# Performance work log

Hardware: AMD Instinct MI355X
Metric: run time of the kernel (lower is better)

Reference implementation:

```python
import jax, jax.numpy as jnp
import numpy as np

# snntorch Leaky defaults / CFG constants
BETA = 0.9      # CFG.lif_beta
IAPP = 0.0      # CFG.Iapp
THR = 1.0       # snn.Leaky default threshold
SLOPE = 25.0    # surrogate.fast_sigmoid default slope


@jax.custom_vjp
def spike(x):
    # Heaviside spike with fast-sigmoid surrogate gradient
    return (x > 0).astype(x.dtype)

def _spike_fwd(x):
    return spike(x), x

def _spike_bwd(x, g):
    return (g / (SLOPE * jnp.abs(x) + 1.0) ** 2,)

spike.defvjp(_spike_fwd, _spike_bwd)


def setup_inputs() -> dict:
    key = jax.random.key(0)
    z = jax.random.normal(key, (32, 1024, 512), dtype=jnp.float32)
    return {"z": z}


def reference(z):
    # z: [B, T, H]; sequential LIF over time axis.
    # snntorch Leaky (reset='subtract'):
    #   reset = detach(V_prev > thr)
    #   V_k   = beta * V_prev + input_k - reset * thr
    #   spk_k = heaviside(V_k - thr)
    # Original loop: input at step k is z[:, k-1] + Iapp (noise std = 0.0).
    B, T, H = z.shape
    zt = jnp.transpose(z[:, :-1, :], (1, 0, 2))  # [T-1, B, H]
    V0 = jnp.zeros((B, H), dtype=z.dtype)

    def step(V, zin):
        reset = jax.lax.stop_gradient((V > THR).astype(V.dtype))
        Vn = BETA * V + (zin + IAPP) - reset * THR
        spk = spike(Vn - THR)
        return Vn, spk

    _, spks = jax.lax.scan(step, V0, zt)  # spks: [T-1, B, H]
    # T[:, 0, :] stays zero (loop starts at k=1)
    Tout = jnp.concatenate(
        [jnp.zeros((B, 1, H), dtype=z.dtype), jnp.transpose(spks, (1, 0, 2))],
        axis=1,
    )
    return Tout
```

## Files before the change

kernel.cpp:

```cpp
#include <hip/hip_runtime.h>


#define LIF_H 512
#define LIF_T 1024
#define CH 128
#define NCH 8
#define NPROD 4
#define NTHREADS (64 * (1 + NPROD))

#define GLDS(gptr, lptr)                                                     \
    __builtin_amdgcn_global_load_lds(                                        \
        (const __attribute__((address_space(1))) void*)(gptr),               \
        (__attribute__((address_space(3))) void*)(lptr), 16, 0, 0)

__global__ __launch_bounds__(NTHREADS, 1) void lif_kernel(const float* __restrict__ z,
                                                          float* __restrict__ out) {
    extern __shared__ float lds[];

    const int tid  = threadIdx.x;
    const int wave = tid >> 6;
    const int lane = tid & 63;
    const int bid  = blockIdx.x;
    const int b    = bid >> 3;
    const int h0   = (bid & 7) << 6;

    const float* zb = z   + b * (LIF_T * LIF_H) + h0;
    float*       ob = out + b * (LIF_T * LIF_H) + h0;

    if (wave == 0) {
        ob[lane] = 0.0f;
    } else {
        const int p = wave - 1;
#pragma unroll
        for (int j = 0; j < 8; ++j) {
            const int r0 = p * 32 + j * 4;
            GLDS(zb + (r0 + (lane >> 4)) * LIF_H + (lane & 15) * 4,
                 &lds[0 * (CH * 64) + r0 * 64]);
        }
#pragma unroll
        for (int j = 0; j < 8; ++j) {
            const int r0 = p * 32 + j * 4;
            GLDS(zb + (CH + r0 + (lane >> 4)) * LIF_H + (lane & 15) * 4,
                 &lds[1 * (CH * 64) + r0 * 64]);
        }
        __builtin_amdgcn_sched_barrier(0);
        asm volatile("s_waitcnt vmcnt(8)" ::: "memory");
    }
    __builtin_amdgcn_s_barrier();

    float V = 0.0f;
    float r = 0.0f;
    int cbuf = 0;

#define LDRB(rb, sub)                                                        \
    _Pragma("unroll")                                                        \
    for (int i = 0; i < 32; ++i) rb[i] = lb[((sub) * 32 + i) * 64 + lane];

#define CHAIN(rb, s0, N)                                                     \
    _Pragma("unroll")                                                        \
    for (int i = 0; i < (N); ++i) {                                          \
        const float u  = __fadd_rn(__fmul_rn(0.9f, V), rb[i]);               \
        const float Vn = __fsub_rn(u, r);                                    \
        const float sp = (Vn > 1.0f) ? 1.0f : 0.0f;                          \
        ob[((s0) + i + 1) * LIF_H + lane] = sp;                              \
        r = sp;                                                              \
        V = Vn;                                                              \
    }

#pragma unroll 1
    for (int c = 0; c < NCH; ++c) {
        if (wave > 0) {
            if (c + 2 < NCH) {
                const int p = wave - 1;
                int wbuf = cbuf + 2; if (wbuf >= 3) wbuf -= 3;
                float* dst = &lds[wbuf * (CH * 64)];
                const float* src = zb + (c + 2) * CH * LIF_H;
#pragma unroll
                for (int j = 0; j < 8; ++j) {
                    const int r0 = p * 32 + j * 4;
                    GLDS(src + (r0 + (lane >> 4)) * LIF_H + (lane & 15) * 4,
                         &dst[r0 * 64]);
                }
                __builtin_amdgcn_sched_barrier(0);
                asm volatile("s_waitcnt vmcnt(8)" ::: "memory");
            } else if (c + 1 < NCH) {
                asm volatile("s_waitcnt vmcnt(0)" ::: "memory");
            }
        } else {
            const float* lb = &lds[cbuf * (CH * 64)];
            const int s0 = c * CH;
            float rbA[32], rbB[32];
            LDRB(rbA, 0);
            LDRB(rbB, 1);
            __builtin_amdgcn_sched_barrier(0);
            CHAIN(rbA, s0 + 0, 32);
            LDRB(rbA, 2);
            __builtin_amdgcn_sched_barrier(0);
            CHAIN(rbB, s0 + 32, 32);
            LDRB(rbB, 3);
            __builtin_amdgcn_sched_barrier(0);
            CHAIN(rbA, s0 + 64, 32);
            __builtin_amdgcn_sched_barrier(0);
            if (c < NCH - 1) {
                CHAIN(rbB, s0 + 96, 32);
            } else {
                CHAIN(rbB, s0 + 96, 31);
            }
        }

        __builtin_amdgcn_s_barrier();
        cbuf = (cbuf == 2) ? 0 : cbuf + 1;
    }
}

extern "C" void kernel_launch(void* const* d_in, const int* in_sizes, int n_in,
                              void* d_out, int out_size, void* d_ws, size_t ws_size,
                              hipStream_t stream) {
    const float* z = (const float*)d_in[0];
    float* out = (float*)d_out;
    hipLaunchKernelGGL(lif_kernel, dim3(256), dim3(NTHREADS),
                       3 * CH * 64 * sizeof(float), stream, z, out);
}
```

Before: 113.4 us.

## Consolidate LIF blocks to 256 columns with four consumer waves and double buffering

Each block now covers 256 hidden columns instead of 64, with four consumer waves and eight producer waves, so the grid drops from 256 blocks to 64. The triple-buffered 128-row LDS pipeline becomes a double-buffered 64-row one, and producers fully drain their loads each phase. The aim is more recurrence chains per CU, fewer loads per thread and simpler buffer rotation. The cost is that three quarters of the CUs sit idle, prefetch runs only one chunk ahead, and there are twice as many block barriers.

Result: slower. 138.7 us (+22.3%).

```diff
diff --git a/kernel.cpp b/kernel.cpp
--- a/kernel.cpp
+++ b/kernel.cpp
@@ -3,10 +3,12 @@
 
 #define LIF_H 512
 #define LIF_T 1024
-#define CH 128
-#define NCH 8
-#define NPROD 4
-#define NTHREADS (64 * (1 + NPROD))
+#define CH 64
+#define NPH 16
+#define NCONS 4
+#define NPROD 8
+#define NTHREADS ((NCONS + NPROD) * 64)
+#define ROWF 256
 
 #define GLDS(gptr, lptr)                                                     \
     __builtin_amdgcn_global_load_lds(                                        \
@@ -21,40 +23,29 @@
     const int wave = tid >> 6;
     const int lane = tid & 63;
     const int bid  = blockIdx.x;
-    const int b    = bid >> 3;
-    const int h0   = (bid & 7) << 6;
+    const int b    = bid >> 1;
+    const int h0   = (bid & 1) << 8;
 
     const float* zb = z   + b * (LIF_T * LIF_H) + h0;
     float*       ob = out + b * (LIF_T * LIF_H) + h0;
 
-    if (wave == 0) {
-        ob[lane] = 0.0f;
+    if (wave < NCONS) {
+        ob[wave * 64 + lane] = 0.0f;
     } else {
-        const int p = wave - 1;
+        const int p = wave - NCONS;
 #pragma unroll
         for (int j = 0; j < 8; ++j) {
-            const int r0 = p * 32 + j * 4;
-            GLDS(zb + (r0 + (lane >> 4)) * LIF_H + (lane & 15) * 4,
-                 &lds[0 * (CH * 64) + r0 * 64]);
-        }
-#pragma unroll
-        for (int j = 0; j < 8; ++j) {
-            const int r0 = p * 32 + j * 4;
-            GLDS(zb + (CH + r0 + (lane >> 4)) * LIF_H + (lane & 15) * 4,
-                 &lds[1 * (CH * 64) + r0 * 64]);
+            const int r = p * 8 + j;
+            GLDS(zb + r * LIF_H + lane * 4, &lds[r * ROWF]);
         }
         __builtin_amdgcn_sched_barrier(0);
-        asm volatile("s_waitcnt vmcnt(8)" ::: "memory");
+        asm volatile("s_waitcnt vmcnt(0)" ::: "memory");
     }
     __builtin_amdgcn_s_barrier();
 
     float V = 0.0f;
     float r = 0.0f;
-    int cbuf = 0;
-
-#define LDRB(rb, sub)                                                        \
-    _Pragma("unroll")                                                        \
-    for (int i = 0; i < 32; ++i) rb[i] = lb[((sub) * 32 + i) * 64 + lane];
+    float* oc = ob + wave * 64 + lane;
 
 #define CHAIN(rb, s0, N)                                                     \
     _Pragma("unroll")                                                        \
@@ -62,54 +53,45 @@
         const float u  = __fadd_rn(__fmul_rn(0.9f, V), rb[i]);               \
         const float Vn = __fsub_rn(u, r);                                    \
         const float sp = (Vn > 1.0f) ? 1.0f : 0.0f;                          \
-        ob[((s0) + i + 1) * LIF_H + lane] = sp;                              \
+        oc[((s0) + i + 1) * LIF_H] = sp;                                     \
         r = sp;                                                              \
         V = Vn;                                                              \
     }
 
 #pragma unroll 1
-    for (int c = 0; c < NCH; ++c) {
-        if (wave > 0) {
-            if (c + 2 < NCH) {
-                const int p = wave - 1;
-                int wbuf = cbuf + 2; if (wbuf >= 3) wbuf -= 3;
-                float* dst = &lds[wbuf * (CH * 64)];
-                const float* src = zb + (c + 2) * CH * LIF_H;
+    for (int c = 0; c < NPH; ++c) {
+        if (wave >= NCONS) {
+            if (c + 1 < NPH) {
+                const int p = wave - NCONS;
+                float* dst = &lds[((c + 1) & 1) * (CH * ROWF)];
+                const float* src = zb + (c + 1) * CH * LIF_H;
 #pragma unroll
                 for (int j = 0; j < 8; ++j) {
-                    const int r0 = p * 32 + j * 4;
-                    GLDS(src + (r0 + (lane >> 4)) * LIF_H + (lane & 15) * 4,
-                         &dst[r0 * 64]);
+                    const int rr = p * 8 + j;
+                    GLDS(src + rr * LIF_H + lane * 4, &dst[rr * ROWF]);
                 }
                 __builtin_amdgcn_sched_barrier(0);
-                asm volatile("s_waitcnt vmcnt(8)" ::: "memory");
-            } else if (c + 1 < NCH) {
                 asm volatile("s_waitcnt vmcnt(0)" ::: "memory");
             }
         } else {
-            const float* lb = &lds[cbuf * (CH * 64)];
+            const float* lb = &lds[(c & 1) * (CH * ROWF)];
+            const int col = wave * 64 + lane;
             const int s0 = c * CH;
             float rbA[32], rbB[32];
-            LDRB(rbA, 0);
-            LDRB(rbB, 1);
+#pragma unroll
+            for (int i = 0; i < 32; ++i) rbA[i] = lb[i * ROWF + col];
+#pragma unroll
+            for (int i = 0; i < 32; ++i) rbB[i] = lb[(32 + i) * ROWF + col];
             __builtin_amdgcn_sched_barrier(0);
-            CHAIN(rbA, s0 + 0, 32);
-            LDRB(rbA, 2);
-            __builtin_amdgcn_sched_barrier(0);
-            CHAIN(rbB, s0 + 32, 32);
-            LDRB(rbB, 3);
-            __builtin_amdgcn_sched_barrier(0);
-            CHAIN(rbA, s0 + 64, 32);
-            __builtin_amdgcn_sched_barrier(0);
-            if (c < NCH - 1) {
-                CHAIN(rbB, s0 + 96, 32);
+            CHAIN(rbA, s0, 32);
+            if (c < NPH - 1) {
+                CHAIN(rbB, s0 + 32, 32);
             } else {
-                CHAIN(rbB, s0 + 96, 31);
+                CHAIN(rbB, s0 + 32, 31);
             }
         }
 
         __builtin_amdgcn_s_barrier();
-        cbuf = (cbuf == 2) ? 0 : cbuf + 1;
     }
 }
 
@@ -118,6 +100,6 @@
                               hipStream_t stream) {
     const float* z = (const float*)d_in[0];
     float* out = (float*)d_out;
-    hipLaunchKernelGGL(lif_kernel, dim3(256), dim3(NTHREADS),
-                       3 * CH * 64 * sizeof(float), stream, z, out);
+    hipLaunchKernelGGL(lif_kernel, dim3(64), dim3(NTHREADS),
+                       2 * CH * ROWF * sizeof(float), stream, z, out);
 }
```

## Write spikes to contiguous workspace then transpose in separate kernel

Applied to the files above, without the earlier changes.

The scan kernel now writes each block's spikes to a private contiguous workspace slab (64 floats per timestep), and a second kernel copies them into the strided output with float4 stores. The goal is to avoid 256-byte strided stores from the serial chain wave. The prefetch is also cut from triple to double buffering with full vmcnt(0) waits. A fallback direct kernel runs when the workspace is too small. The extra kernel adds a full 64 MB read-plus-write round trip and a launch, and the shallower prefetch may expose load latency.

Measured after the change: 132.3 us. 16.6% more time.

```diff
diff --git a/kernel.cpp b/kernel.cpp
--- a/kernel.cpp
+++ b/kernel.cpp
@@ -7,15 +7,16 @@
 #define NCH 8
 #define NPROD 4
 #define NTHREADS (64 * (1 + NPROD))
+#define WS_FLOATS (256ull * LIF_T * 64)
 
 #define GLDS(gptr, lptr)                                                     \
     __builtin_amdgcn_global_load_lds(                                        \
         (const __attribute__((address_space(1))) void*)(gptr),               \
         (__attribute__((address_space(3))) void*)(lptr), 16, 0, 0)
 
-__global__ __launch_bounds__(NTHREADS, 1) void lif_kernel(const float* __restrict__ z,
-                                                          float* __restrict__ out) {
-    extern __shared__ float lds[];
+__global__ __launch_bounds__(NTHREADS, 1) void lif_scan(const float* __restrict__ z,
+                                                        float* __restrict__ ws) {
+    __shared__ float lds[2][CH * 64];
 
     const int tid  = threadIdx.x;
     const int wave = tid >> 6;
@@ -24,6 +25,109 @@
     const int b    = bid >> 3;
     const int h0   = (bid & 7) << 6;
 
+    const float* zb  = z  + b * (LIF_T * LIF_H) + h0;
+    float*       wsb = ws + (size_t)bid * (LIF_T * 64);
+
+    if (wave == 0) {
+        wsb[lane] = 0.0f;
+    } else {
+        const int p = wave - 1;
+#pragma unroll
+        for (int j = 0; j < 8; ++j) {
+            const int r0 = p * 32 + j * 4;
+            GLDS(zb + (r0 + (lane >> 4)) * LIF_H + (lane & 15) * 4,
+                 &lds[0][r0 * 64]);
+        }
+        __builtin_amdgcn_sched_barrier(0);
+        asm volatile("s_waitcnt vmcnt(0)" ::: "memory");
+    }
+    __builtin_amdgcn_s_barrier();
+
+    float V = 0.0f;
+    float r = 0.0f;
+
+#define LDRB(rb, sub)                                                        \
+    _Pragma("unroll")                                                        \
+    for (int i = 0; i < 32; ++i) rb[i] = lb[((sub) * 32 + i) * 64 + lane];
+
+#define CHAINW(rb, s0, N)                                                    \
+    _Pragma("unroll")                                                        \
+    for (int i = 0; i < (N); ++i) {                                          \
+        const float u  = __fadd_rn(__fmul_rn(0.9f, V), rb[i]);               \
+        const float Vn = __fsub_rn(u, r);                                    \
+        const float sp = (Vn > 1.0f) ? 1.0f : 0.0f;                          \
+        wsb[((s0) + i + 1) * 64 + lane] = sp;                                \
+        r = sp;                                                              \
+        V = Vn;                                                              \
+    }
+
+#pragma unroll 1
+    for (int c = 0; c < NCH; ++c) {
+        if (wave > 0) {
+            if (c + 1 < NCH) {
+                const int p = wave - 1;
+                float* dst = lds[(c + 1) & 1];
+                const float* src = zb + (c + 1) * CH * LIF_H;
+#pragma unroll
+                for (int j = 0; j < 8; ++j) {
+                    const int r0 = p * 32 + j * 4;
+                    GLDS(src + (r0 + (lane >> 4)) * LIF_H + (lane & 15) * 4,
+                         &dst[r0 * 64]);
+                }
+                __builtin_amdgcn_sched_barrier(0);
+                asm volatile("s_waitcnt vmcnt(0)" ::: "memory");
+            }
+        } else {
+            const float* lb = lds[c & 1];
+            const int s0 = c * CH;
+            float rbA[32], rbB[32];
+            LDRB(rbA, 0);
+            LDRB(rbB, 1);
+            __builtin_amdgcn_sched_barrier(0);
+            CHAINW(rbA, s0 + 0, 32);
+            LDRB(rbA, 2);
+            __builtin_amdgcn_sched_barrier(0);
+            CHAINW(rbB, s0 + 32, 32);
+            LDRB(rbB, 3);
+            __builtin_amdgcn_sched_barrier(0);
+            CHAINW(rbA, s0 + 64, 32);
+            __builtin_amdgcn_sched_barrier(0);
+            if (c < NCH - 1) {
+                CHAINW(rbB, s0 + 96, 32);
+            } else {
+                CHAINW(rbB, s0 + 96, 31);
+            }
+        }
+        __builtin_amdgcn_s_barrier();
+    }
+}
+
+__global__ __launch_bounds__(256, 1) void lif_transpose(const float* __restrict__ ws,
+                                                        float* __restrict__ out) {
+    const int gid = blockIdx.x * 256 + threadIdx.x;
+    const int b   = gid >> 17;
+    const int rem = gid & 131071;
+    const int t   = rem >> 7;
+    const int h4  = rem & 127;
+    const int s   = h4 >> 4;
+    const int c4  = h4 & 15;
+    const float4 v = *reinterpret_cast<const float4*>(
+        ws + ((size_t)(b * 8 + s) * (LIF_T * 64) + t * 64 + c4 * 4));
+    *reinterpret_cast<float4*>(
+        out + ((size_t)b * (LIF_T * LIF_H) + (size_t)t * LIF_H + h4 * 4)) = v;
+}
+
+__global__ __launch_bounds__(NTHREADS, 1) void lif_direct(const float* __restrict__ z,
+                                                          float* __restrict__ out) {
+    __shared__ float lds[2][CH * 64];
+
+    const int tid  = threadIdx.x;
+    const int wave = tid >> 6;
+    const int lane = tid & 63;
+    const int bid  = blockIdx.x;
+    const int b    = bid >> 3;
+    const int h0   = (bid & 7) << 6;
+
     const float* zb = z   + b * (LIF_T * LIF_H) + h0;
     float*       ob = out + b * (LIF_T * LIF_H) + h0;
 
@@ -35,28 +139,17 @@
         for (int j = 0; j < 8; ++j) {
             const int r0 = p * 32 + j * 4;
             GLDS(zb + (r0 + (lane >> 4)) * LIF_H + (lane & 15) * 4,
-                 &lds[0 * (CH * 64) + r0 * 64]);
-        }
-#pragma unroll
-        for (int j = 0; j < 8; ++j) {
-            const int r0 = p * 32 + j * 4;
-            GLDS(zb + (CH + r0 + (lane >> 4)) * LIF_H + (lane & 15) * 4,
-                 &lds[1 * (CH * 64) + r0 * 64]);
+                 &lds[0][r0 * 64]);
         }
         __builtin_amdgcn_sched_barrier(0);
-        asm volatile("s_waitcnt vmcnt(8)" ::: "memory");
+        asm volatile("s_waitcnt vmcnt(0)" ::: "memory");
     }
     __builtin_amdgcn_s_barrier();
 
     float V = 0.0f;
     float r = 0.0f;
-    int cbuf = 0;
-
-#define LDRB(rb, sub)                                                        \
-    _Pragma("unroll")                                                        \
-    for (int i = 0; i < 32; ++i) rb[i] = lb[((sub) * 32 + i) * 64 + lane];
-
-#define CHAIN(rb, s0, N)                                                     \
+
+#define CHAIND(rb, s0, N)                                                    \
     _Pragma("unroll")                                                        \
     for (int i = 0; i < (N); ++i) {                                          \
         const float u  = __fadd_rn(__fmul_rn(0.9f, V), rb[i]);               \
@@ -70,11 +163,10 @@
 #pragma unroll 1
     for (int c = 0; c < NCH; ++c) {
         if (wave > 0) {
-            if (c + 2 < NCH) {
+            if (c + 1 < NCH) {
                 const int p = wave - 1;
-                int wbuf = cbuf + 2; if (wbuf >= 3) wbuf -= 3;
-                float* dst = &lds[wbuf * (CH * 64)];
-                const float* src = zb + (c + 2) * CH * LIF_H;
+                float* dst = lds[(c + 1) & 1];
+                const float* src = zb + (c + 1) * CH * LIF_H;
 #pragma unroll
                 for (int j = 0; j < 8; ++j) {
                     const int r0 = p * 32 + j * 4;
@@ -82,34 +174,30 @@
                          &dst[r0 * 64]);
                 }
                 __builtin_amdgcn_sched_barrier(0);
-                asm volatile("s_waitcnt vmcnt(8)" ::: "memory");
-            } else if (c + 1 < NCH) {
                 asm volatile("s_waitcnt vmcnt(0)" ::: "memory");
             }
         } else {
-            const float* lb = &lds[cbuf * (CH * 64)];
+            const float* lb = lds[c & 1];
             const int s0 = c * CH;
             float rbA[32], rbB[32];
             LDRB(rbA, 0);
             LDRB(rbB, 1);
             __builtin_amdgcn_sched_barrier(0);
-            CHAIN(rbA, s0 + 0, 32);
+            CHAIND(rbA, s0 + 0, 32);
             LDRB(rbA, 2);
             __builtin_amdgcn_sched_barrier(0);
-            CHAIN(rbB, s0 + 32, 32);
+            CHAIND(rbB, s0 + 32, 32);
             LDRB(rbB, 3);
             __builtin_amdgcn_sched_barrier(0);
-            CHAIN(rbA, s0 + 64, 32);
+            CHAIND(rbA, s0 + 64, 32);
             __builtin_amdgcn_sched_barrier(0);
             if (c < NCH - 1) {
-                CHAIN(rbB, s0 + 96, 32);
+                CHAIND(rbB, s0 + 96, 32);
             } else {
-                CHAIN(rbB, s0 + 96, 31);
-            }
-        }
-
+                CHAIND(rbB, s0 + 96, 31);
+            }
+        }
         __builtin_amdgcn_s_barrier();
-        cbuf = (cbuf == 2) ? 0 : cbuf + 1;
     }
 }
 
@@ -118,6 +206,11 @@
                               hipStream_t stream) {
     const float* z = (const float*)d_in[0];
     float* out = (float*)d_out;
-    hipLaunchKernelGGL(lif_kernel, dim3(256), dim3(NTHREADS),
-                       3 * CH * 64 * sizeof(float), stream, z, out);
-}
+    if (ws_size >= WS_FLOATS * sizeof(float)) {
+        float* ws = (float*)d_ws;
+        hipLaunchKernelGGL(lif_scan, dim3(256), dim3(NTHREADS), 0, stream, z, ws);
+        hipLaunchKernelGGL(lif_transpose, dim3(16384), dim3(256), 0, stream, ws, out);
+    } else {
+        hipLaunchKernelGGL(lif_direct, dim3(256), dim3(NTHREADS), 0, stream, z, out);
+    }
+}
```

## Split time axis into segments chained through workspace flags

Applied to the files above, without the earlier changes.

Replaces the per-(batch, column-slice) kernel with blocks that each own one 128-step time segment across all 512 columns. A block waits on an agent-scope flag until the previous segment's block publishes its final membrane state, then continues the recurrence from it, so input loading for later segments overlaps with earlier ones. A memset of the flags is added before launch. If the workspace is too small, a simplified double-buffered direct kernel runs instead. This relies on all blocks being co-resident, otherwise the spin-wait can deadlock, and it serialises the chain across segments.

New measurement: 229.2 us. 102% more time.

```diff
diff --git a/kernel.cpp b/kernel.cpp
--- a/kernel.cpp
+++ b/kernel.cpp
@@ -3,19 +3,136 @@
 
 #define LIF_H 512
 #define LIF_T 1024
-#define CH 128
-#define NCH 8
-#define NPROD 4
-#define NTHREADS (64 * (1 + NPROD))
+#define NSEG 8
+#define SEGT 128
+#define SUBT 32
+#define NSUB 4
+#define NCONS 8
+#define NPROD 8
+#define NTHREADS ((NCONS + NPROD) * 64)
+#define BUF_FLOATS (SUBT * LIF_H)
+#define VBUF_FLOATS (32 * NSEG * LIF_H)
+#define VBUF_BYTES (VBUF_FLOATS * sizeof(float))
+#define FLAG_BYTES (32 * NSEG * sizeof(int))
+#define WS_NEED (VBUF_BYTES + FLAG_BYTES)
 
 #define GLDS(gptr, lptr)                                                     \
     __builtin_amdgcn_global_load_lds(                                        \
         (const __attribute__((address_space(1))) void*)(gptr),               \
         (__attribute__((address_space(3))) void*)(lptr), 16, 0, 0)
 
-__global__ __launch_bounds__(NTHREADS, 1) void lif_kernel(const float* __restrict__ z,
-                                                          float* __restrict__ out) {
+__global__ __launch_bounds__(NTHREADS, 1) void lif_seg(const float* __restrict__ z,
+                                                       float* __restrict__ out,
+                                                       float* __restrict__ vbuf,
+                                                       int* __restrict__ flags) {
     extern __shared__ float lds[];
+
+    const int tid  = threadIdx.x;
+    const int wave = tid >> 6;
+    const int lane = tid & 63;
+    const int bid  = blockIdx.x;
+    const int b    = bid & 31;
+    const int seg  = bid >> 5;
+
+    const float* zs = z + (size_t)b * (LIF_T * LIF_H) + (size_t)seg * SEGT * LIF_H;
+    float*       ob = out + (size_t)b * (LIF_T * LIF_H);
+    const int col = (wave & 7) * 64 + lane;
+
+    float V = 0.0f;
+    float r = 0.0f;
+
+    if (wave >= NCONS) {
+        const int p = wave - NCONS;
+#pragma unroll
+        for (int j = 0; j < 8; ++j)
+            GLDS(zs + (p * 8 + j) * 256 + lane * 4, &lds[(p * 8 + j) * 256]);
+#pragma unroll
+        for (int j = 0; j < 8; ++j)
+            GLDS(zs + SUBT * LIF_H + (p * 8 + j) * 256 + lane * 4,
+                 &lds[BUF_FLOATS + (p * 8 + j) * 256]);
+        __builtin_amdgcn_sched_barrier(0);
+        asm volatile("s_waitcnt vmcnt(8)" ::: "memory");
+    } else {
+        if (seg == 0) {
+            ob[col] = 0.0f;
+        } else {
+            const int fi = (seg - 1) * 32 + b;
+            while (__hip_atomic_load(&flags[fi], __ATOMIC_RELAXED,
+                                     __HIP_MEMORY_SCOPE_AGENT) < NCONS)
+                __builtin_amdgcn_s_sleep(2);
+            __builtin_amdgcn_fence(__ATOMIC_ACQUIRE, "agent");
+            V = vbuf[(size_t)fi * LIF_H + col];
+            r = (V > 1.0f) ? 1.0f : 0.0f;
+        }
+    }
+    __builtin_amdgcn_s_barrier();
+
+#define CHAIN(N)                                                             \
+    _Pragma("unroll")                                                        \
+    for (int i = 0; i < (N); ++i) {                                          \
+        const float u  = __fadd_rn(__fmul_rn(0.9f, V), rb[i]);               \
+        const float Vn = __fsub_rn(u, r);                                    \
+        const float sp = (Vn > 1.0f) ? 1.0f : 0.0f;                          \
+        ob[(size_t)(s0 + i + 1) * LIF_H + col] = sp;                         \
+        r = sp;                                                              \
+        V = Vn;                                                              \
+    }
+
+#pragma unroll 1
+    for (int c = 0; c < NSUB; ++c) {
+        float rb[SUBT];
+        if (wave < NCONS) {
+            const float* lb = &lds[(c & 1) * BUF_FLOATS];
+#pragma unroll
+            for (int i = 0; i < SUBT; ++i) rb[i] = lb[i * LIF_H + col];
+            asm volatile("s_waitcnt lgkmcnt(0)" ::: "memory");
+            __builtin_amdgcn_sched_barrier(0);
+        }
+        __builtin_amdgcn_s_barrier();
+
+        if (wave < NCONS) {
+            const int s0 = seg * SEGT + c * SUBT;
+            if (seg == NSEG - 1 && c == NSUB - 1) {
+                CHAIN(SUBT - 1);
+            } else {
+                CHAIN(SUBT);
+            }
+        } else {
+            const int p = wave - NCONS;
+            if (c + 2 < NSUB) {
+                const float* src = zs + (size_t)(c + 2) * SUBT * LIF_H;
+                float* dst = &lds[(c & 1) * BUF_FLOATS];
+#pragma unroll
+                for (int j = 0; j < 8; ++j)
+                    GLDS(src + (p * 8 + j) * 256 + lane * 4,
+                         &dst[(p * 8 + j) * 256]);
+                __builtin_amdgcn_sched_barrier(0);
+                asm volatile("s_waitcnt vmcnt(8)" ::: "memory");
+            } else if (c + 2 == NSUB) {
+                asm volatile("s_waitcnt vmcnt(0)" ::: "memory");
+            }
+        }
+        __builtin_amdgcn_s_barrier();
+    }
+
+    if (wave < NCONS && seg < NSEG - 1) {
+        const int fi = seg * 32 + b;
+        vbuf[(size_t)fi * LIF_H + col] = V;
+        asm volatile("s_waitcnt vmcnt(0)" ::: "memory");
+        if (lane == 0)
+            __hip_atomic_fetch_add(&flags[fi], 1, __ATOMIC_RELEASE,
+                                   __HIP_MEMORY_SCOPE_AGENT);
+    }
+#undef CHAIN
+}
+
+#define CH 128
+#define FNPROD 4
+#define FNTHREADS (64 * (1 + FNPROD))
+
+__global__ __launch_bounds__(FNTHREADS, 1) void lif_direct(const float* __restrict__ z,
+                                                           float* __restrict__ out) {
+    __shared__ float slds[2][CH * 64];
 
     const int tid  = threadIdx.x;
     const int wave = tid >> 6;
@@ -35,28 +152,20 @@
         for (int j = 0; j < 8; ++j) {
             const int r0 = p * 32 + j * 4;
             GLDS(zb + (r0 + (lane >> 4)) * LIF_H + (lane & 15) * 4,
-                 &lds[0 * (CH * 64) + r0 * 64]);
-        }
-#pragma unroll
-        for (int j = 0; j < 8; ++j) {
-            const int r0 = p * 32 + j * 4;
-            GLDS(zb + (CH + r0 + (lane >> 4)) * LIF_H + (lane & 15) * 4,
-                 &lds[1 * (CH * 64) + r0 * 64]);
+                 &slds[0][r0 * 64]);
         }
         __builtin_amdgcn_sched_barrier(0);
-        asm volatile("s_waitcnt vmcnt(8)" ::: "memory");
+        asm volatile("s_waitcnt vmcnt(0)" ::: "memory");
     }
     __builtin_amdgcn_s_barrier();
 
-    float V = 0.0f;
-    float r = 0.0f;
-    int cbuf = 0;
+    float V = 0.0f, r = 0.0f;
 
 #define LDRB(rb, sub)                                                        \
     _Pragma("unroll")                                                        \
     for (int i = 0; i < 32; ++i) rb[i] = lb[((sub) * 32 + i) * 64 + lane];
 
-#define CHAIN(rb, s0, N)                                                     \
+#define CHAIND(rb, s0, N)                                                    \
     _Pragma("unroll")                                                        \
     for (int i = 0; i < (N); ++i) {                                          \
         const float u  = __fadd_rn(__fmul_rn(0.9f, V), rb[i]);               \
@@ -68,13 +177,12 @@
     }
 
 #pragma unroll 1
-    for (int c = 0; c < NCH; ++c) {
+    for (int c = 0; c < 8; ++c) {
         if (wave > 0) {
-            if (c + 2 < NCH) {
+            if (c + 1 < 8) {
                 const int p = wave - 1;
-                int wbuf = cbuf + 2; if (wbuf >= 3) wbuf -= 3;
-                float* dst = &lds[wbuf * (CH * 64)];
-                const float* src = zb + (c + 2) * CH * LIF_H;
+                float* dst = slds[(c + 1) & 1];
+                const float* src = zb + (c + 1) * CH * LIF_H;
 #pragma unroll
                 for (int j = 0; j < 8; ++j) {
                     const int r0 = p * 32 + j * 4;
@@ -82,34 +190,30 @@
                          &dst[r0 * 64]);
                 }
                 __builtin_amdgcn_sched_barrier(0);
-                asm volatile("s_waitcnt vmcnt(8)" ::: "memory");
-            } else if (c + 1 < NCH) {
                 asm volatile("s_waitcnt vmcnt(0)" ::: "memory");
             }
         } else {
-            const float* lb = &lds[cbuf * (CH * 64)];
+            const float* lb = slds[c & 1];
             const int s0 = c * CH;
             float rbA[32], rbB[32];
             LDRB(rbA, 0);
             LDRB(rbB, 1);
             __builtin_amdgcn_sched_barrier(0);
-            CHAIN(rbA, s0 + 0, 32);
+            CHAIND(rbA, s0 + 0, 32);
             LDRB(rbA, 2);
             __builtin_amdgcn_sched_barrier(0);
-            CHAIN(rbB, s0 + 32, 32);
+            CHAIND(rbB, s0 + 32, 32);
             LDRB(rbB, 3);
             __builtin_amdgcn_sched_barrier(0);
-            CHAIN(rbA, s0 + 64, 32);
-            __builtin_amdgcn_sched_barrier(0);
-            if (c < NCH - 1) {
-                CHAIN(rbB, s0 + 96, 32);
+            CHAIND(rbA, s0 + 64, 32);
+            __builtin_amdgcn_sched_barrier(0);
+            if (c < 7) {
+                CHAIND(rbB, s0 + 96, 32);
             } else {
-                CHAIN(rbB, s0 + 96, 31);
-            }
-        }
-
+                CHAIND(rbB, s0 + 96, 31);
+            }
+        }
         __builtin_amdgcn_s_barrier();
-        cbuf = (cbuf == 2) ? 0 : cbuf + 1;
     }
 }
 
@@ -118,6 +222,14 @@
                               hipStream_t stream) {
     const float* z = (const float*)d_in[0];
     float* out = (float*)d_out;
-    hipLaunchKernelGGL(lif_kernel, dim3(256), dim3(NTHREADS),
-                       3 * CH * 64 * sizeof(float), stream, z, out);
+    if (ws_size >= WS_NEED) {
+        float* vbuf = (float*)d_ws;
+        int* flags = (int*)((char*)d_ws + VBUF_BYTES);
+        hipMemsetAsync(flags, 0, FLAG_BYTES, stream);
+        hipLaunchKernelGGL(lif_seg, dim3(256), dim3(NTHREADS),
+                           2 * BUF_FLOATS * sizeof(float), stream,
+                           z, out, vbuf, flags);
+    } else {
+        hipLaunchKernelGGL(lif_direct, dim3(256), dim3(FNTHREADS), 0, stream, z, out);
+    }
 }
```
